# Performance work log

Measured on AMD Instinct MI355X. Metric: run time of the kernel, lower is better.

Reference implementation:

```python
import jax, jax.numpy as jnp
import numpy as np

EMBED_DIM = 1024
NUM_HEADS = 16
HEAD_DIM = EMBED_DIM // NUM_HEADS
ROPE_THETA = 10000.0


def setup_inputs() -> dict:
    key = jax.random.key(0)
    k1, k2, k3, k4, k5 = jax.random.split(key, 5)
    B, S, E = 2, 2048, EMBED_DIM
    scale = 1.0 / np.sqrt(E)
    x = jax.random.normal(k1, (B, S, E), dtype=jnp.float32)
    w_qkv = jax.random.normal(k2, (E, 3 * E), dtype=jnp.float32) * scale
    b_qkv = jnp.zeros((3 * E,), dtype=jnp.float32)
    w_o = jax.random.normal(k3, (E, E), dtype=jnp.float32) * scale
    b_o = jnp.zeros((E,), dtype=jnp.float32)
    return {"x": x, "w_qkv": w_qkv, "b_qkv": b_qkv, "w_o": w_o, "b_o": b_o}


def _rope_cos_sin(seq_len, dtype):
    # half-dim frequencies, GPT-NeoX rotate-half convention
    inv_freq = 1.0 / (ROPE_THETA ** (jnp.arange(0, HEAD_DIM, 2, dtype=jnp.float32) / HEAD_DIM))
    pos = jnp.arange(seq_len, dtype=jnp.float32)
    freqs = pos[:, None] * inv_freq[None, :]          # [S, hd/2]
    emb = jnp.concatenate([freqs, freqs], axis=-1)    # [S, hd]
    return jnp.cos(emb).astype(dtype), jnp.sin(emb).astype(dtype)


def _rotate_half(t):
    t1, t2 = jnp.split(t, 2, axis=-1)
    return jnp.concatenate([-t2, t1], axis=-1)


def reference(x, w_qkv, b_qkv, w_o, b_o):
    B, S, E = x.shape
    H, D = NUM_HEADS, HEAD_DIM
    qkv = x @ w_qkv + b_qkv                            # [B, S, 3E]
    q, k, v = jnp.split(qkv, 3, axis=-1)
    # [B, H, S, D]
    q = q.reshape(B, S, H, D).transpose(0, 2, 1, 3)
    k = k.reshape(B, S, H, D).transpose(0, 2, 1, 3)
    v = v.reshape(B, S, H, D).transpose(0, 2, 1, 3)
    cos, sin = _rope_cos_sin(S, x.dtype)               # [S, D]
    q = q * cos + _rotate_half(q) * sin
    k = k * cos + _rotate_half(k) * sin
    scores = jnp.einsum('bhqd,bhkd->bhqk', q, k) / jnp.sqrt(jnp.asarray(D, x.dtype))
    causal = jnp.tril(jnp.ones((S, S), dtype=bool))
    scores = jnp.where(causal, scores, jnp.asarray(-1e30, x.dtype))
    attn = jax.nn.softmax(scores, axis=-1)
    out = jnp.einsum('bhqk,bhkd->bhqd', attn, v)       # [B, H, S, D]
    out = out.transpose(0, 2, 1, 3).reshape(B, S, E)
    return out @ w_o + b_o
```

## Files before the change

### kernel.cpp

```cpp
#include <hip/hip_runtime.h>
#include <hip/hip_bf16.h>

typedef __hip_bfloat16 bf16_t;
typedef __attribute__((ext_vector_type(8))) __bf16 bf16x8;
typedef __attribute__((ext_vector_type(4))) float f32x4;
typedef __attribute__((ext_vector_type(4))) unsigned short ushort4v;

#define NUM_B 2
#define NUM_H 16
#define SEQ   2048
#define EMB   1024
#define LOG2E 1.44269504088896340736f

__global__ void cast_f32_bf16_kernel(const float* __restrict__ src,
                                     bf16_t* __restrict__ dst) {
  int i = (blockIdx.x * 256 + threadIdx.x) * 4;
  f32x4 v = *(const f32x4*)&src[i];
  ushort4v p;
#pragma unroll
  for (int j = 0; j < 4; ++j)
    p[j] = __builtin_bit_cast(unsigned short, __float2bfloat16(v[j]));
  *(ushort4v*)&dst[i] = p;
}

__global__ void transpose_cast_kernel(const float* __restrict__ src,
                                      bf16_t* __restrict__ dst, int R, int C) {
  __shared__ float tile[32][33];
  int c0 = blockIdx.x * 32, r0 = blockIdx.y * 32;
  int tx = threadIdx.x & 31, ty = threadIdx.x >> 5;
#pragma unroll
  for (int i = 0; i < 4; ++i)
    tile[ty + i * 8][tx] = src[(size_t)(r0 + ty + i * 8) * C + c0 + tx];
  __syncthreads();
#pragma unroll
  for (int i = 0; i < 4; ++i)
    dst[(size_t)(c0 + ty + i * 8) * R + r0 + tx] = __float2bfloat16(tile[tx][ty + i * 8]);
}

__device__ __forceinline__ void stage_tile(const bf16_t* __restrict__ G,
                                           int row0, int col0, int ld,
                                           bf16_t* Ls, int wave, int lane) {
  int c0 = wave * 64 + lane;
  const char* g0 = (const char*)(G + (size_t)(row0 + (c0 >> 2)) * ld + col0) + (c0 & 3) * 16;
  char* l0 = (char*)Ls + c0 * 16;
  __builtin_amdgcn_global_load_lds((const __attribute__((address_space(1))) void*)g0,
                                   (__attribute__((address_space(3))) void*)l0, 16, 0, 0);
  int c1 = c0 + 256;
  const char* g1 = (const char*)(G + (size_t)(row0 + (c1 >> 2)) * ld + col0) + (c1 & 3) * 16;
  char* l1 = (char*)Ls + c1 * 16;
  __builtin_amdgcn_global_load_lds((const __attribute__((address_space(1))) void*)g1,
                                   (__attribute__((address_space(3))) void*)l1, 16, 0, 0);
}

template <int MODE>
__global__ __launch_bounds__(256) void gemm_bf16_kernel(
    const bf16_t* __restrict__ A, const bf16_t* __restrict__ Bt,
    const float* __restrict__ bias, bf16_t* __restrict__ out0,
    bf16_t* __restrict__ out1, bf16_t* __restrict__ out2,
    float* __restrict__ outf, int Ndim, int Kdim) {
  __shared__ __align__(16) bf16_t As[128 * 32];
  __shared__ __align__(16) bf16_t Bs[128 * 32];
  int tid = threadIdx.x;
  int wave = tid >> 6, lane = tid & 63;
  int lr = lane & 15, lq = lane >> 4;
  int m0 = blockIdx.x * 128, n0 = blockIdx.y * 128;
  int wm = (wave >> 1) * 64, wn = (wave & 1) * 64;
  f32x4 acc[4][4];
#pragma unroll
  for (int i = 0; i < 4; ++i)
#pragma unroll
    for (int j = 0; j < 4; ++j) acc[i][j] = (f32x4){0.f, 0.f, 0.f, 0.f};

  for (int k0 = 0; k0 < Kdim; k0 += 32) {
    __syncthreads();
    stage_tile(A, m0, k0, Kdim, As, wave, lane);
    stage_tile(Bt, n0, k0, Kdim, Bs, wave, lane);
    __syncthreads();
    bf16x8 af[4], bfr[4];
#pragma unroll
    for (int mt = 0; mt < 4; ++mt)
      af[mt] = *(const bf16x8*)&As[(wm + mt * 16 + lr) * 32 + lq * 8];
#pragma unroll
    for (int nt = 0; nt < 4; ++nt)
      bfr[nt] = *(const bf16x8*)&Bs[(wn + nt * 16 + lr) * 32 + lq * 8];
#pragma unroll
    for (int mt = 0; mt < 4; ++mt)
#pragma unroll
      for (int nt = 0; nt < 4; ++nt)
        acc[mt][nt] = __builtin_amdgcn_mfma_f32_16x16x32_bf16(af[mt], bfr[nt], acc[mt][nt], 0, 0, 0);
  }

#pragma unroll
  for (int nt = 0; nt < 4; ++nt) {
    int n = n0 + wn + nt * 16 + lr;
    float bv = bias[n];
    if (MODE == 0) {
      int sec = n >> 10;
      int h = (n >> 6) & (NUM_H - 1);
      int d = n & 63;
#pragma unroll
      for (int mt = 0; mt < 4; ++mt) {
        int mbase = m0 + wm + mt * 16 + lq * 4;
        int b = mbase >> 11;
        int s = mbase & (SEQ - 1);
        int bh = b * NUM_H + h;
        if (sec == 2) {
          ushort4v pk;
#pragma unroll
          for (int r = 0; r < 4; ++r)
            pk[r] = __builtin_bit_cast(unsigned short, __float2bfloat16(acc[mt][nt][r] + bv));
          *(ushort4v*)&out2[((size_t)bh * 64 + d) * SEQ + s] = pk;
        } else {
          bf16_t* dst = (sec == 0) ? out0 : out1;
#pragma unroll
          for (int r = 0; r < 4; ++r)
            dst[((size_t)bh * SEQ + (s + r)) * 64 + d] = __float2bfloat16(acc[mt][nt][r] + bv);
        }
      }
    } else {
#pragma unroll
      for (int mt = 0; mt < 4; ++mt)
#pragma unroll
        for (int r = 0; r < 4; ++r) {
          int m = m0 + wm + mt * 16 + lq * 4 + r;
          outf[(size_t)m * Ndim + n] = acc[mt][nt][r] + bv;
        }
    }
  }
}

__global__ void rope_kernel(bf16_t* __restrict__ Q, bf16_t* __restrict__ K) {
  int idx = blockIdx.x * blockDim.x + threadIdx.x;
  int i = idx & 31;
  int bhs = idx >> 5;
  int s = bhs & (SEQ - 1);
  float inv = exp2f(-(float)i * (13.287712379549449f / 32.0f));
  float f = (float)s * inv;
  float sn, cs;
  sincosf(f, &sn, &cs);
  size_t base = (size_t)bhs * 64;
  float q1 = __bfloat162float(Q[base + i]);
  float q2 = __bfloat162float(Q[base + i + 32]);
  float k1 = __bfloat162float(K[base + i]);
  float k2 = __bfloat162float(K[base + i + 32]);
  Q[base + i]      = __float2bfloat16((q1 * cs - q2 * sn) * 0.125f);
  Q[base + i + 32] = __float2bfloat16((q2 * cs + q1 * sn) * 0.125f);
  K[base + i]      = __float2bfloat16(k1 * cs - k2 * sn);
  K[base + i + 32] = __float2bfloat16(k2 * cs + k1 * sn);
}

__device__ __forceinline__ void stage_sw(const char* __restrict__ gbase,
                                         size_t rowStride, bf16_t* lds, int tid) {
#pragma unroll
  for (int r = 0; r < 2; ++r) {
    int c = tid + r * 256;
    int row = c >> 3, g = c & 7;
    const char* gp = gbase + (size_t)row * rowStride + ((g ^ (row & 7)) * 16);
    char* lp = (char*)lds + c * 16;
    __builtin_amdgcn_global_load_lds((const __attribute__((address_space(1))) void*)gp,
                                     (__attribute__((address_space(3))) void*)lp, 16, 0, 0);
  }
}

__global__ __launch_bounds__(256) void flash_attn_kernel(
    const bf16_t* __restrict__ Q, const bf16_t* __restrict__ K,
    const bf16_t* __restrict__ Vt, bf16_t* __restrict__ O) {
  __shared__ __align__(16) bf16_t Ks[64 * 64];
  __shared__ __align__(16) bf16_t Vs[64 * 64];
  __shared__ __align__(16) bf16_t Psh[4][16 * 68];
  int tid = threadIdx.x;
  int wv = tid >> 6, lane = tid & 63;
  int lr = lane & 15, lq = lane >> 4;
  int bx = blockIdx.x;
  int bh = bx & 31;
  int pair = bx >> 5;
  const bf16_t* Qb = Q + (size_t)bh * SEQ * 64;
  const bf16_t* Kb = K + (size_t)bh * SEQ * 64;
  const bf16_t* Vb = Vt + (size_t)bh * 64 * SEQ;
  bf16_t* Pw = Psh[wv];
  int sw = lr & 7;
  int g0 = (lq ^ sw) * 8;
  int g1 = g0 ^ 32;

#pragma unroll
  for (int ti = 0; ti < 2; ++ti) {
    int tile = (ti == 0) ? (31 - pair) : pair;
    int qw0 = tile * 64 + wv * 16;

    bf16x8 aq0 = *(const bf16x8*)&Qb[(size_t)(qw0 + lr) * 64 + lq * 8];
    bf16x8 aq1 = *(const bf16x8*)&Qb[(size_t)(qw0 + lr) * 64 + 32 + lq * 8];

    f32x4 Oacc[4];
#pragma unroll
    for (int dt = 0; dt < 4; ++dt) Oacc[dt] = (f32x4){0.f, 0.f, 0.f, 0.f};
    float lrow = 0.f;

    for (int ch = 0; ch <= tile; ++ch) {
      int kv0 = ch * 64;
      bool diag = (ch == tile);

      __syncthreads();
      stage_sw((const char*)(Kb + (size_t)kv0 * 64), 128, Ks, tid);
      stage_sw((const char*)Vb + (size_t)kv0 * 2, SEQ * 2, Vs, tid);
      __syncthreads();

#pragma unroll
      for (int sub = 0; sub < 4; ++sub) {
        ushort4v pk;
        if (!diag || sub <= wv) {
          int rk = (sub * 16 + lr) * 64;
          bf16x8 k0 = *(const bf16x8*)&Ks[rk + g0];
          bf16x8 k1 = *(const bf16x8*)&Ks[rk + g1];
          f32x4 t = (f32x4){0.f, 0.f, 0.f, 0.f};
          t = __builtin_amdgcn_mfma_f32_16x16x32_bf16(k0, aq0, t, 0, 0, 0);
          t = __builtin_amdgcn_mfma_f32_16x16x32_bf16(k1, aq1, t, 0, 0, 0);
          if (diag && sub == wv) {
#pragma unroll
            for (int r = 0; r < 4; ++r)
              if (lq * 4 + r > lr) t[r] = -1e30f;
          }
#pragma unroll
          for (int r = 0; r < 4; ++r) {
            float p = exp2f(t[r] * LOG2E);
            lrow += p;
            pk[r] = __builtin_bit_cast(unsigned short, __float2bfloat16(p));
          }
        } else {
          pk = (ushort4v){0, 0, 0, 0};
        }
        *(ushort4v*)&Pw[lr * 68 + sub * 16 + lq * 4] = pk;
      }

      bf16x8 ap0 = *(const bf16x8*)&Pw[lr * 68 + lq * 8];
      bf16x8 ap1 = *(const bf16x8*)&Pw[lr * 68 + 32 + lq * 8];
#pragma unroll
      for (int dt = 0; dt < 4; ++dt) {
        int rv = (dt * 16 + lr) * 64;
        bf16x8 v0 = *(const bf16x8*)&Vs[rv + g0];
        bf16x8 v1 = *(const bf16x8*)&Vs[rv + g1];
        Oacc[dt] = __builtin_amdgcn_mfma_f32_16x16x32_bf16(v0, ap0, Oacc[dt], 0, 0, 0);
        Oacc[dt] = __builtin_amdgcn_mfma_f32_16x16x32_bf16(v1, ap1, Oacc[dt], 0, 0, 0);
      }
    }

    lrow += __shfl_xor(lrow, 16, 64);
    lrow += __shfl_xor(lrow, 32, 64);

    int b = bh >> 4, h = bh & (NUM_H - 1);
    int q = qw0 + lr;
    size_t base = (((size_t)b * SEQ + q) * NUM_H + h) * 64;
    float rinv = 1.0f / lrow;
#pragma unroll
    for (int dt = 0; dt < 4; ++dt) {
      ushort4v ok;
#pragma unroll
      for (int r = 0; r < 4; ++r)
        ok[r] = __builtin_bit_cast(unsigned short, __float2bfloat16(Oacc[dt][r] * rinv));
      *(ushort4v*)&O[base + dt * 16 + lq * 4] = ok;
    }
  }
}

extern "C" void kernel_launch(void* const* d_in, const int* in_sizes, int n_in,
                              void* d_out, int out_size, void* d_ws, size_t ws_size,
                              hipStream_t stream) {
  const float* x      = (const float*)d_in[0];
  const float* w_qkv  = (const float*)d_in[1];
  const float* b_qkv  = (const float*)d_in[2];
  const float* w_o    = (const float*)d_in[3];
  const float* b_o    = (const float*)d_in[4];
  float* out = (float*)d_out;

  bf16_t* ws    = (bf16_t*)d_ws;
  bf16_t* xb    = ws;
  bf16_t* wqkvT = xb + 4 * 1024 * 1024;
  bf16_t* woT   = wqkvT + 3072 * 1024;
  bf16_t* Qb    = woT + 1024 * 1024;
  bf16_t* Kb    = Qb + 4 * 1024 * 1024;
  bf16_t* Vt    = Kb + 4 * 1024 * 1024;
  bf16_t* attn  = Vt + 4 * 1024 * 1024;

  cast_f32_bf16_kernel<<<4096, 256, 0, stream>>>(x, xb);
  transpose_cast_kernel<<<dim3(96, 32), 256, 0, stream>>>(w_qkv, wqkvT, 1024, 3072);
  transpose_cast_kernel<<<dim3(32, 32), 256, 0, stream>>>(w_o, woT, 1024, 1024);
  gemm_bf16_kernel<0><<<dim3(32, 24), 256, 0, stream>>>(xb, wqkvT, b_qkv, Qb, Kb, Vt, nullptr, 3072, 1024);
  rope_kernel<<<8192, 256, 0, stream>>>(Qb, Kb);
  flash_attn_kernel<<<512, 256, 0, stream>>>(Qb, Kb, Vt, attn);
  gemm_bf16_kernel<1><<<dim3(32, 8), 256, 0, stream>>>(attn, woT, b_o, nullptr, nullptr, nullptr, out, 1024, 1024);
}
```

Measured before the change: 211.9 us.

## Fuse RoPE into QKV GEMM epilogue and double-buffer K/V tiles in attention

Applies the rotary embedding and Q scaling inside the QKV GEMM epilogue by pairing accumulator columns d and d+32 held by the same lane, and removes the separate rope kernel with its read-modify-write pass over Q and K. The flash attention kernel now double-buffers K/V shared-memory tiles so the next chunk's async global-to-LDS load is issued before computing on the current one, with one barrier per chunk instead of two. This costs extra sincos work in the GEMM epilogue and doubles LDS for K/V, which may lower occupancy. The single barrier per chunk relies on the async LDS loads being complete by the next iteration's sync.

```diff
diff --git a/kernel.cpp b/kernel.cpp
--- a/kernel.cpp
+++ b/kernel.cpp
@@ -11,6 +11,7 @@
 #define SEQ   2048
 #define EMB   1024
 #define LOG2E 1.44269504088896340736f
+#define LN10K 13.287712379549449f
 
 __global__ void cast_f32_bf16_kernel(const float* __restrict__ src,
                                      bf16_t* __restrict__ dst) {
@@ -90,34 +91,62 @@
         acc[mt][nt] = __builtin_amdgcn_mfma_f32_16x16x32_bf16(af[mt], bfr[nt], acc[mt][nt], 0, 0, 0);
   }
 
-#pragma unroll
-  for (int nt = 0; nt < 4; ++nt) {
-    int n = n0 + wn + nt * 16 + lr;
-    float bv = bias[n];
-    if (MODE == 0) {
-      int sec = n >> 10;
-      int h = (n >> 6) & (NUM_H - 1);
-      int d = n & 63;
-#pragma unroll
-      for (int mt = 0; mt < 4; ++mt) {
-        int mbase = m0 + wm + mt * 16 + lq * 4;
-        int b = mbase >> 11;
-        int s = mbase & (SEQ - 1);
-        int bh = b * NUM_H + h;
-        if (sec == 2) {
-          ushort4v pk;
-#pragma unroll
-          for (int r = 0; r < 4; ++r)
-            pk[r] = __builtin_bit_cast(unsigned short, __float2bfloat16(acc[mt][nt][r] + bv));
-          *(ushort4v*)&out2[((size_t)bh * 64 + d) * SEQ + s] = pk;
-        } else {
-          bf16_t* dst = (sec == 0) ? out0 : out1;
-#pragma unroll
-          for (int r = 0; r < 4; ++r)
-            dst[((size_t)bh * SEQ + (s + r)) * 64 + d] = __float2bfloat16(acc[mt][nt][r] + bv);
+  if (MODE == 0) {
+#pragma unroll
+    for (int pr = 0; pr < 2; ++pr) {
+      int na = n0 + wn + pr * 16 + lr;
+      int nb = na + 32;
+      int sec = na >> 10;
+      int h = (na >> 6) & (NUM_H - 1);
+      int da = na & 63;
+      float bva = bias[na], bvb = bias[nb];
+      if (sec == 2) {
+#pragma unroll
+        for (int mt = 0; mt < 4; ++mt) {
+          int mbase = m0 + wm + mt * 16 + lq * 4;
+          int b = mbase >> 11;
+          int s = mbase & (SEQ - 1);
+          int bh = b * NUM_H + h;
+          ushort4v pa, pb;
+#pragma unroll
+          for (int r = 0; r < 4; ++r) {
+            pa[r] = __builtin_bit_cast(unsigned short, __float2bfloat16(acc[mt][pr][r] + bva));
+            pb[r] = __builtin_bit_cast(unsigned short, __float2bfloat16(acc[mt][pr + 2][r] + bvb));
+          }
+          *(ushort4v*)&out2[((size_t)bh * 64 + da) * SEQ + s] = pa;
+          *(ushort4v*)&out2[((size_t)bh * 64 + da + 32) * SEQ + s] = pb;
+        }
+      } else {
+        bf16_t* dst = (sec == 0) ? out0 : out1;
+        float scale = (sec == 0) ? 0.125f : 1.0f;
+        int i = da & 31;
+        float inv = exp2f(-(float)i * (LN10K / 32.0f));
+#pragma unroll
+        for (int mt = 0; mt < 4; ++mt) {
+          int mbase = m0 + wm + mt * 16 + lq * 4;
+          int b = mbase >> 11;
+          int s0 = mbase & (SEQ - 1);
+          int bh = b * NUM_H + h;
+#pragma unroll
+          for (int r = 0; r < 4; ++r) {
+            float sn, cs;
+            sincosf((float)(s0 + r) * inv, &sn, &cs);
+            float va = acc[mt][pr][r] + bva;
+            float vb = acc[mt][pr + 2][r] + bvb;
+            float oa = (va * cs - vb * sn) * scale;
+            float ob = (vb * cs + va * sn) * scale;
+            size_t rowb = ((size_t)bh * SEQ + (s0 + r)) * 64;
+            dst[rowb + da] = __float2bfloat16(oa);
+            dst[rowb + da + 32] = __float2bfloat16(ob);
+          }
         }
       }
-    } else {
+    }
+  } else {
+#pragma unroll
+    for (int nt = 0; nt < 4; ++nt) {
+      int n = n0 + wn + nt * 16 + lr;
+      float bv = bias[n];
 #pragma unroll
       for (int mt = 0; mt < 4; ++mt)
 #pragma unroll
@@ -127,26 +156,6 @@
         }
     }
   }
-}
-
-__global__ void rope_kernel(bf16_t* __restrict__ Q, bf16_t* __restrict__ K) {
-  int idx = blockIdx.x * blockDim.x + threadIdx.x;
-  int i = idx & 31;
-  int bhs = idx >> 5;
-  int s = bhs & (SEQ - 1);
-  float inv = exp2f(-(float)i * (13.287712379549449f / 32.0f));
-  float f = (float)s * inv;
-  float sn, cs;
-  sincosf(f, &sn, &cs);
-  size_t base = (size_t)bhs * 64;
-  float q1 = __bfloat162float(Q[base + i]);
-  float q2 = __bfloat162float(Q[base + i + 32]);
-  float k1 = __bfloat162float(K[base + i]);
-  float k2 = __bfloat162float(K[base + i + 32]);
-  Q[base + i]      = __float2bfloat16((q1 * cs - q2 * sn) * 0.125f);
-  Q[base + i + 32] = __float2bfloat16((q2 * cs + q1 * sn) * 0.125f);
-  K[base + i]      = __float2bfloat16(k1 * cs - k2 * sn);
-  K[base + i + 32] = __float2bfloat16(k2 * cs + k1 * sn);
 }
 
 __device__ __forceinline__ void stage_sw(const char* __restrict__ gbase,
@@ -165,8 +174,8 @@
 __global__ __launch_bounds__(256) void flash_attn_kernel(
     const bf16_t* __restrict__ Q, const bf16_t* __restrict__ K,
     const bf16_t* __restrict__ Vt, bf16_t* __restrict__ O) {
-  __shared__ __align__(16) bf16_t Ks[64 * 64];
-  __shared__ __align__(16) bf16_t Vs[64 * 64];
+  __shared__ __align__(16) bf16_t Ks[2][64 * 64];
+  __shared__ __align__(16) bf16_t Vs[2][64 * 64];
   __shared__ __align__(16) bf16_t Psh[4][16 * 68];
   int tid = threadIdx.x;
   int wv = tid >> 6, lane = tid & 63;
@@ -195,22 +204,28 @@
     for (int dt = 0; dt < 4; ++dt) Oacc[dt] = (f32x4){0.f, 0.f, 0.f, 0.f};
     float lrow = 0.f;
 
-    for (int ch = 0; ch <= tile; ++ch) {
-      int kv0 = ch * 64;
+    int nch = tile + 1;
+    __syncthreads();
+    stage_sw((const char*)Kb, 128, Ks[0], tid);
+    stage_sw((const char*)Vb, SEQ * 2, Vs[0], tid);
+
+    for (int ch = 0; ch < nch; ++ch) {
+      int cur = ch & 1;
       bool diag = (ch == tile);
-
       __syncthreads();
-      stage_sw((const char*)(Kb + (size_t)kv0 * 64), 128, Ks, tid);
-      stage_sw((const char*)Vb + (size_t)kv0 * 2, SEQ * 2, Vs, tid);
-      __syncthreads();
+      if (ch + 1 < nch) {
+        int kvn = (ch + 1) * 64;
+        stage_sw((const char*)(Kb + (size_t)kvn * 64), 128, Ks[cur ^ 1], tid);
+        stage_sw((const char*)Vb + (size_t)kvn * 2, SEQ * 2, Vs[cur ^ 1], tid);
+      }
 
 #pragma unroll
       for (int sub = 0; sub < 4; ++sub) {
         ushort4v pk;
         if (!diag || sub <= wv) {
           int rk = (sub * 16 + lr) * 64;
-          bf16x8 k0 = *(const bf16x8*)&Ks[rk + g0];
-          bf16x8 k1 = *(const bf16x8*)&Ks[rk + g1];
+          bf16x8 k0 = *(const bf16x8*)&Ks[cur][rk + g0];
+          bf16x8 k1 = *(const bf16x8*)&Ks[cur][rk + g1];
           f32x4 t = (f32x4){0.f, 0.f, 0.f, 0.f};
           t = __builtin_amdgcn_mfma_f32_16x16x32_bf16(k0, aq0, t, 0, 0, 0);
           t = __builtin_amdgcn_mfma_f32_16x16x32_bf16(k1, aq1, t, 0, 0, 0);
@@ -236,8 +251,8 @@
 #pragma unroll
       for (int dt = 0; dt < 4; ++dt) {
         int rv = (dt * 16 + lr) * 64;
-        bf16x8 v0 = *(const bf16x8*)&Vs[rv + g0];
-        bf16x8 v1 = *(const bf16x8*)&Vs[rv + g1];
+        bf16x8 v0 = *(const bf16x8*)&Vs[cur][rv + g0];
+        bf16x8 v1 = *(const bf16x8*)&Vs[cur][rv + g1];
         Oacc[dt] = __builtin_amdgcn_mfma_f32_16x16x32_bf16(v0, ap0, Oacc[dt], 0, 0, 0);
         Oacc[dt] = __builtin_amdgcn_mfma_f32_16x16x32_bf16(v1, ap1, Oacc[dt], 0, 0, 0);
       }
@@ -284,7 +299,6 @@
   transpose_cast_kernel<<<dim3(96, 32), 256, 0, stream>>>(w_qkv, wqkvT, 1024, 3072);
   transpose_cast_kernel<<<dim3(32, 32), 256, 0, stream>>>(w_o, woT, 1024, 1024);
   gemm_bf16_kernel<0><<<dim3(32, 24), 256, 0, stream>>>(xb, wqkvT, b_qkv, Qb, Kb, Vt, nullptr, 3072, 1024);
-  rope_kernel<<<8192, 256, 0, stream>>>(Qb, Kb);
   flash_attn_kernel<<<512, 256, 0, stream>>>(Qb, Kb, Vt, attn);
   gemm_bf16_kernel<1><<<dim3(32, 8), 256, 0, stream>>>(attn, woT, b_o, nullptr, nullptr, nullptr, out, 1024, 1024);
 }
```

Measured after the change: 201.7 us. -4.9%, faster.
